# Optimization experiments

Measured on AMD Instinct MI355X. Metric: run time of the kernel, lower is better.

## Reference

```python
import jax, jax.numpy as jnp
import numpy as np

N_NODES = 50000
N_EDGES = 400000
IN_CH = 109
OUT_CH = 32


def setup_inputs() -> dict:
    key = jax.random.key(0)
    ks = jax.random.split(key, 12)
    dims = [(IN_CH, 10 * OUT_CH), (10 * OUT_CH, 2 * OUT_CH), (2 * OUT_CH, OUT_CH), (2 * OUT_CH, OUT_CH)]
    inp = {
        'x': jax.random.normal(ks[0], (N_NODES, IN_CH), dtype=jnp.float32),
        'edge_index': jax.random.randint(ks[1], (2, N_EDGES), 0, N_NODES, dtype=jnp.int64) if jax.config.jax_enable_x64 else jax.random.randint(ks[1], (2, N_EDGES), 0, N_NODES, dtype=jnp.int32),
    }
    names = ['W1', 'b1', 'W2', 'b2', 'Wmu', 'bmu', 'Wls', 'bls']
    for i, (fi, fo) in enumerate(dims):
        scale = 1.0 / np.sqrt(fi)
        inp[names[2 * i]] = jax.random.uniform(ks[2 + 2 * i], (fi, fo), minval=-scale, maxval=scale, dtype=jnp.float32)
        inp[names[2 * i + 1]] = jnp.zeros((fo,), dtype=jnp.float32)
    return inp


def _gcn_conv(x, src, dst, norm, W, b, n):
    # PyG GCNConv: h = x @ W, then symmetric-normalized aggregation, then + b
    h = x @ W                                   # [N, F_out]
    msg = h[src] * norm[:, None]                # [E+N, F_out]
    out = jax.ops.segment_sum(msg, dst, num_segments=n)
    return out + b


def _norm_and_loops(edge_index, n):
    # add self loops, compute D^{-1/2}(A+I)D^{-1/2} edge weights
    loops = jnp.arange(n, dtype=edge_index.dtype)
    src = jnp.concatenate([edge_index[0], loops])
    dst = jnp.concatenate([edge_index[1], loops])
    deg = jax.ops.segment_sum(jnp.ones_like(src, dtype=jnp.float32), dst, num_segments=n)
    dinv = jnp.where(deg > 0, jax.lax.rsqrt(jnp.maximum(deg, 1.0)), 0.0)
    norm = dinv[src] * dinv[dst]
    return src, dst, norm


def reference(x, edge_index, W1, b1, W2, b2, Wmu, bmu, Wls, bls):
    n = x.shape[0]
    src, dst, norm = _norm_and_loops(edge_index, n)
    h = jax.nn.relu(_gcn_conv(x, src, dst, norm, W1, b1, n))
    h = jax.nn.relu(_gcn_conv(h, src, dst, norm, W2, b2, n))
    mu = _gcn_conv(h, src, dst, norm, Wmu, bmu, n)
    logstd = _gcn_conv(h, src, dst, norm, Wls, bls, n)
    return (mu, logstd)
```

## Files before the change

kernel.cpp:

```cpp
#include <hip/hip_runtime.h>

#define NN 50000
#define NE 400000

typedef __attribute__((ext_vector_type(8))) short short8v;
typedef __attribute__((ext_vector_type(4))) float f32x4;

__device__ __forceinline__ unsigned short f2bf_rtn(float x) {
    unsigned u = __float_as_uint(x);
    unsigned r = u + 0x7FFFu + ((u >> 16) & 1u);
    return (unsigned short)(r >> 16);
}
__device__ __forceinline__ float bf2f(unsigned short h) {
    return __uint_as_float(((unsigned)h) << 16);
}

__global__ void prep_kernel(const float* __restrict__ x,
                            const float* __restrict__ W1, const float* __restrict__ W2,
                            const float* __restrict__ Wmu, const float* __restrict__ Wls,
                            unsigned* __restrict__ xp, int* __restrict__ zero_base,
                            unsigned short* __restrict__ w1t_hi,
                            unsigned short* __restrict__ w2t_hi,
                            unsigned short* __restrict__ wct_hi) {
    int b = blockIdx.x, tid = threadIdx.x;
    if (b < 12500) {
        int idx = b * 256 + tid;
        int i = idx >> 6, c2 = (idx & 63) * 2;
        long xb = (long)i * 109;
        float v0 = (c2 < 109) ? x[xb + c2] : 0.0f;
        float v1 = (c2 + 1 < 109) ? x[xb + c2 + 1] : 0.0f;
        xp[idx] = (unsigned)f2bf_rtn(v0) | ((unsigned)f2bf_rtn(v1) << 16);
    } else if (b < 12891) {
        int i = (b - 12500) * 256 + tid;
        if (i < 100096) zero_base[i] = 0;
    } else if (b < 13051) {
        int idx = (b - 12891) * 256 + tid;
        int n = idx >> 7, k = idx & 127;
        float v = (k < 109) ? W1[(long)k * 320 + n] : 0.0f;
        w1t_hi[idx] = f2bf_rtn(v);
    } else if (b < 13131) {
        int idx = (b - 13051) * 256 + tid;
        int n = idx / 320, k = idx - n * 320;
        w2t_hi[idx] = f2bf_rtn(W2[(long)k * 64 + n]);
    } else {
        int idx = (b - 13131) * 256 + tid;
        int n = idx >> 6, k = idx & 63;
        float v = (n < 32) ? Wmu[k * 32 + n] : Wls[k * 32 + (n - 32)];
        wct_hi[idx] = f2bf_rtn(v);
    }
}

__global__ void hist_kernel(const int* __restrict__ dst, int* __restrict__ counts) {
    for (int e = blockIdx.x * blockDim.x + threadIdx.x; e < NE; e += gridDim.x * blockDim.x)
        atomicAdd(&counts[dst[e]], 1);
}

__global__ void dinv_scan1_kernel(const int* __restrict__ counts, float* __restrict__ dinv,
                                  int* __restrict__ rowstart, int* __restrict__ bsum) {
    __shared__ int tmp[256];
    int tid = threadIdx.x;
    int i = blockIdx.x * 256 + tid;
    int v = (i < NN) ? counts[i] : 0;
    if (i < NN) dinv[i] = rsqrtf((float)(v + 1));
    tmp[tid] = v;
    __syncthreads();
    for (int off = 1; off < 256; off <<= 1) {
        int t = 0;
        if (tid >= off) t = tmp[tid - off];
        __syncthreads();
        if (tid >= off) tmp[tid] += t;
        __syncthreads();
    }
    if (i < NN) rowstart[i] = tmp[tid] - v;
    if (tid == 255) bsum[blockIdx.x] = tmp[255];
}

__global__ void scan23_kernel(int* __restrict__ rowstart, const int* __restrict__ bsum) {
    __shared__ int red[4];
    int tid = threadIdx.x;
    int v = (tid < 196 && tid < (int)blockIdx.x) ? bsum[tid] : 0;
    for (int off = 32; off > 0; off >>= 1) v += __shfl_down(v, off, 64);
    if ((tid & 63) == 0) red[tid >> 6] = v;
    __syncthreads();
    int pref = red[0] + red[1] + red[2] + red[3];
    int i = blockIdx.x * 256 + tid;
    if (i < NN) rowstart[i] += pref;
    if (i == 0) rowstart[NN] = NE;
}

__global__ void scatter_kernel(const int* __restrict__ src, const int* __restrict__ dst,
                               const int* __restrict__ rowstart, int* __restrict__ cursor,
                               int* __restrict__ esrc) {
    for (int e = blockIdx.x * blockDim.x + threadIdx.x; e < NE; e += gridDim.x * blockDim.x) {
        int d = dst[e];
        int pos = rowstart[d] + atomicAdd(&cursor[d], 1);
        esrc[pos] = src[e];
    }
}

__global__ __launch_bounds__(256) void agg109_packed_kernel(const int* __restrict__ rowstart,
                                                            const int* __restrict__ esrc,
                                                            const float* __restrict__ dinv,
                                                            const unsigned* __restrict__ xp,
                                                            unsigned* __restrict__ xa_hi32) {
    int wave = blockIdx.x * (blockDim.x >> 6) + (threadIdx.x >> 6);
    if (wave >= NN) return;
    int lane = threadIdx.x & 63;
    float wd = dinv[wave];
    unsigned pself = xp[(long)wave * 64 + lane];
    float acc0 = __uint_as_float(pself << 16) * wd;
    float acc1 = __uint_as_float(pself & 0xFFFF0000u) * wd;
    int j0 = rowstart[wave], j1 = rowstart[wave + 1];
    int j = j0;
    for (; j + 8 <= j1; j += 8) {
        int s[8];
        float w[8];
        unsigned pp[8];
        #pragma unroll
        for (int u = 0; u < 8; ++u) s[u] = esrc[j + u];
        #pragma unroll
        for (int u = 0; u < 8; ++u) w[u] = dinv[s[u]];
        #pragma unroll
        for (int u = 0; u < 8; ++u) pp[u] = xp[(long)s[u] * 64 + lane];
        #pragma unroll
        for (int u = 0; u < 8; ++u) {
            acc0 = fmaf(__uint_as_float(pp[u] << 16), w[u], acc0);
            acc1 = fmaf(__uint_as_float(pp[u] & 0xFFFF0000u), w[u], acc1);
        }
    }
    for (; j + 4 <= j1; j += 4) {
        int s0 = esrc[j], s1 = esrc[j + 1], s2 = esrc[j + 2], s3 = esrc[j + 3];
        float w0 = dinv[s0], w1 = dinv[s1], w2 = dinv[s2], w3 = dinv[s3];
        unsigned p0 = xp[(long)s0 * 64 + lane], p1 = xp[(long)s1 * 64 + lane];
        unsigned p2 = xp[(long)s2 * 64 + lane], p3 = xp[(long)s3 * 64 + lane];
        acc0 = fmaf(__uint_as_float(p0 << 16), w0, acc0);
        acc1 = fmaf(__uint_as_float(p0 & 0xFFFF0000u), w0, acc1);
        acc0 = fmaf(__uint_as_float(p1 << 16), w1, acc0);
        acc1 = fmaf(__uint_as_float(p1 & 0xFFFF0000u), w1, acc1);
        acc0 = fmaf(__uint_as_float(p2 << 16), w2, acc0);
        acc1 = fmaf(__uint_as_float(p2 & 0xFFFF0000u), w2, acc1);
        acc0 = fmaf(__uint_as_float(p3 << 16), w3, acc0);
        acc1 = fmaf(__uint_as_float(p3 & 0xFFFF0000u), w3, acc1);
    }
    for (; j < j1; ++j) {
        int s = esrc[j];
        float w = dinv[s];
        unsigned pv = xp[(long)s * 64 + lane];
        acc0 = fmaf(__uint_as_float(pv << 16), w, acc0);
        acc1 = fmaf(__uint_as_float(pv & 0xFFFF0000u), w, acc1);
    }
    acc0 *= wd;
    acc1 *= wd;
    xa_hi32[(long)wave * 64 + lane] =
        (unsigned)f2bf_rtn(acc0) | ((unsigned)f2bf_rtn(acc1) << 16);
}

__global__ __launch_bounds__(256) void agg64_relu_bf16_kernel(const int* __restrict__ rowstart,
                                                              const int* __restrict__ esrc,
                                                              const float* __restrict__ dinv,
                                                              const unsigned short* __restrict__ g,
                                                              const float* __restrict__ b,
                                                              unsigned short* __restrict__ hhi) {
    int wave = blockIdx.x * (blockDim.x >> 6) + (threadIdx.x >> 6);
    if (wave >= NN) return;
    int lane = threadIdx.x & 63;
    long base = (long)wave * 64;
    float acc = bf2f(g[base + lane]);
    int j0 = rowstart[wave], j1 = rowstart[wave + 1];
    int j = j0;
    for (; j + 8 <= j1; j += 8) {
        int s[8];
        float pp[8];
        #pragma unroll
        for (int u = 0; u < 8; ++u) s[u] = esrc[j + u];
        #pragma unroll
        for (int u = 0; u < 8; ++u) pp[u] = bf2f(g[(long)s[u] * 64 + lane]);
        #pragma unroll
        for (int u = 0; u < 8; ++u) acc += pp[u];
    }
    for (; j + 4 <= j1; j += 4) {
        int s0 = esrc[j], s1 = esrc[j + 1], s2 = esrc[j + 2], s3 = esrc[j + 3];
        float p0 = bf2f(g[(long)s0 * 64 + lane]), p1 = bf2f(g[(long)s1 * 64 + lane]);
        float p2 = bf2f(g[(long)s2 * 64 + lane]), p3 = bf2f(g[(long)s3 * 64 + lane]);
        acc += p0 + p1 + p2 + p3;
    }
    for (; j < j1; ++j) acc += bf2f(g[(long)esrc[j] * 64 + lane]);
    float v = acc * dinv[wave] + b[lane];
    v = v > 0.0f ? v : 0.0f;
    hhi[base + lane] = f2bf_rtn(v);
}

#define LDT 72
__global__ __launch_bounds__(1024) void agg_gemm3_kernel(const int* __restrict__ rowstart,
                                                         const int* __restrict__ esrc,
                                                         const float* __restrict__ dinv,
                                                         const unsigned short* __restrict__ h,
                                                         const unsigned short* __restrict__ wct_hi,
                                                         const float* __restrict__ bmu,
                                                         const float* __restrict__ bls,
                                                         float* __restrict__ out) {
    __shared__ unsigned short As[64 * LDT];
    __shared__ unsigned short Bs[64 * LDT];
    int tid = threadIdx.x;
    int wid = tid >> 6, lane = tid & 63;
    int m0 = blockIdx.x * 64;

    if (tid < 512) {
        int row = tid >> 3, slot = tid & 7;
        *(uint4*)&Bs[row * LDT + slot * 8] = *(const uint4*)&wct_hi[row * 64 + slot * 8];
    }

    #pragma unroll
    for (int t = 0; t < 4; ++t) {
        int node = m0 + wid * 4 + t;
        int i = node < NN ? node : NN - 1;
        long base = (long)i * 64;
        float wd = dinv[i];
        float acc = bf2f(h[base + lane]) * wd;
        int j0 = rowstart[i], j1 = rowstart[i + 1];
        int j = j0;
        for (; j + 8 <= j1; j += 8) {
            int s[8];
            float w[8], pp[8];
            #pragma unroll
            for (int u = 0; u < 8; ++u) s[u] = esrc[j + u];
            #pragma unroll
            for (int u = 0; u < 8; ++u) w[u] = dinv[s[u]];
            #pragma unroll
            for (int u = 0; u < 8; ++u) pp[u] = bf2f(h[(long)s[u] * 64 + lane]);
            #pragma unroll
            for (int u = 0; u < 8; ++u) acc = fmaf(pp[u], w[u], acc);
        }
        for (; j + 4 <= j1; j += 4) {
            int s0 = esrc[j], s1 = esrc[j + 1], s2 = esrc[j + 2], s3 = esrc[j + 3];
            float w0 = dinv[s0], w1 = dinv[s1], w2 = dinv[s2], w3 = dinv[s3];
            float p0 = bf2f(h[(long)s0 * 64 + lane]), p1 = bf2f(h[(long)s1 * 64 + lane]);
            float p2 = bf2f(h[(long)s2 * 64 + lane]), p3 = bf2f(h[(long)s3 * 64 + lane]);
            acc = fmaf(p0, w0, acc); acc = fmaf(p1, w1, acc);
            acc = fmaf(p2, w2, acc); acc = fmaf(p3, w3, acc);
        }
        for (; j < j1; ++j) {
            int s = esrc[j];
            acc = fmaf(bf2f(h[(long)s * 64 + lane]), dinv[s], acc);
        }
        As[(wid * 4 + t) * LDT + lane] = f2bf_rtn(acc * wd);
    }
    __syncthreads();

    int r = wid >> 2, c = wid & 3;
    int l15 = lane & 15, l4 = lane >> 4;
    f32x4 acc4 = {};
    #pragma unroll
    for (int ks = 0; ks < 2; ++ks) {
        int koff = ks * 32 + l4 * 8;
        short8v ah = *(const short8v*)&As[(r * 16 + l15) * LDT + koff];
        short8v bh = *(const short8v*)&Bs[(c * 16 + l15) * LDT + koff];
        acc4 = __builtin_amdgcn_mfma_f32_16x16x32_bf16(ah, bh, acc4, 0, 0, 0);
    }
    int rbase = m0 + r * 16 + l4 * 4;
    int gcol = c * 16 + l15;
    #pragma unroll
    for (int q2 = 0; q2 < 4; ++q2) {
        int grow = rbase + q2;
        if (grow >= NN) continue;
        float v = acc4[q2];
        if (gcol < 32)
            out[(long)grow * 32 + gcol] = v + bmu[gcol];
        else
            out[(long)NN * 32 + (long)grow * 32 + (gcol - 32)] = v + bls[gcol - 32];
    }
}

template <int MODE>
__global__ __launch_bounds__(256) void mfma_gemm_kernel(
    const unsigned short* __restrict__ Ahi,
    const unsigned short* __restrict__ Bhi,
    const float* __restrict__ bias,
    const float* __restrict__ dinv,
    unsigned short* __restrict__ Chi, int M, int N, int K, int grid_n) {
    __shared__ unsigned short As[64 * LDT];
    __shared__ unsigned short Bs[64 * LDT];
    int tid = threadIdx.x;
    int wid = tid >> 6, lane = tid & 63;
    int l15 = lane & 15, l4 = lane >> 4;

    int T = gridDim.x;
    int xcd = blockIdx.x & 7, jj = blockIdx.x >> 3;
    int q = T >> 3, r = T & 7;
    int start = (xcd < r) ? xcd * (q + 1) : r * (q + 1) + (xcd - r) * q;
    int lin = start + jj;
    int bm = lin / grid_n, bn = lin - bm * grid_n;
    int bm0 = bm * 64, bn0 = bn * 64;

    f32x4 acc[4] = {};

    for (int kc = 0; kc < K; kc += 64) {
        #pragma unroll
        for (int r2 = 0; r2 < 2; ++r2) {
            int idx = tid + 256 * r2;
            int row = idx >> 3, slot = idx & 7;
            int grow = bm0 + row;
            if (grow >= M) grow = M - 1;
            long go = (long)grow * K + kc + slot * 8;
            *(uint4*)&As[row * LDT + slot * 8] = *(const uint4*)&Ahi[go];
            long gob = (long)(bn0 + row) * K + kc + slot * 8;
            *(uint4*)&Bs[row * LDT + slot * 8] = *(const uint4*)&Bhi[gob];
        }
        __syncthreads();
        #pragma unroll
        for (int ks = 0; ks < 2; ++ks) {
            int koff = ks * 32 + l4 * 8;
            int ra = (wid * 16 + l15) * LDT + koff;
            short8v ah = *(const short8v*)&As[ra];
            #pragma unroll
            for (int n = 0; n < 4; ++n) {
                int rb = (n * 16 + l15) * LDT + koff;
                short8v bh = *(const short8v*)&Bs[rb];
                acc[n] = __builtin_amdgcn_mfma_f32_16x16x32_bf16(ah, bh, acc[n], 0, 0, 0);
            }
        }
        __syncthreads();
    }
    int rbase = bm0 + wid * 16 + l4 * 4;
    #pragma unroll
    for (int q2 = 0; q2 < 4; ++q2) {
        int grow = rbase + q2;
        if (grow >= M) continue;
        float rs = (MODE == 1) ? dinv[grow] : 0.0f;
        #pragma unroll
        for (int n = 0; n < 4; ++n) {
            int gcol = bn0 + n * 16 + l15;
            float v = acc[n][q2];
            if (MODE == 0) {
                v += bias[gcol];
                v = v > 0.0f ? v : 0.0f;
                Chi[(long)grow * N + gcol] = f2bf_rtn(v);
            } else {
                Chi[(long)grow * N + gcol] = f2bf_rtn(v * rs);
            }
        }
    }
}

extern "C" void kernel_launch(void* const* d_in, const int* in_sizes, int n_in,
                              void* d_out, int out_size, void* d_ws, size_t ws_size,
                              hipStream_t stream) {
    const float* x   = (const float*)d_in[0];
    const int*   ei  = (const int*)d_in[1];
    const int*   src = ei;
    const int*   dst = ei + NE;
    const float* W1  = (const float*)d_in[2];
    const float* b1  = (const float*)d_in[3];
    const float* W2  = (const float*)d_in[4];
    const float* b2  = (const float*)d_in[5];
    const float* Wmu = (const float*)d_in[6];
    const float* bmu = (const float*)d_in[7];
    const float* Wls = (const float*)d_in[8];
    const float* bls = (const float*)d_in[9];
    float* out = (float*)d_out;

    char* p = (char*)d_ws;
    float* dinv   = (float*)p; p += 50048 * 4;
    int* counts   = (int*)p;   p += 50048 * 4;
    int* cursor   = (int*)p;   p += 50048 * 4;
    int* rowstart = (int*)p;   p += 50056 * 4;
    int* bsum     = (int*)p;   p += 256 * 4;
    int* esrc     = (int*)p;   p += 400000 * 4;
    unsigned* xp          = (unsigned*)p;       p += 50000L * 64 * 4;
    unsigned short* xa_hi = (unsigned short*)p; p += 50000L * 128 * 2;
    unsigned short* g2b   = (unsigned short*)p; p += 50000L * 64 * 2;
    unsigned short* h1_hi = (unsigned short*)p; p += 50000L * 320 * 2;
    unsigned short* w1t_hi = (unsigned short*)p; p += 320 * 128 * 2;
    unsigned short* w2t_hi = (unsigned short*)p; p += 64 * 320 * 2;
    unsigned short* wct_hi = (unsigned short*)p; p += 64 * 64 * 2;
    unsigned short* h2_hi = xa_hi;

    const int TB = 256;
    const int NB_NODES = (NN + TB - 1) / TB;
    const int NB_AGG = (NN * 64 + TB - 1) / TB;

    prep_kernel<<<13147, TB, 0, stream>>>(x, W1, W2, Wmu, Wls, xp, counts,
                                          w1t_hi, w2t_hi, wct_hi);
    hist_kernel<<<1024, TB, 0, stream>>>(dst, counts);
    dinv_scan1_kernel<<<NB_NODES, TB, 0, stream>>>(counts, dinv, rowstart, bsum);
    scan23_kernel<<<NB_NODES, TB, 0, stream>>>(rowstart, bsum);
    scatter_kernel<<<1024, TB, 0, stream>>>(src, dst, rowstart, cursor, esrc);

    agg109_packed_kernel<<<NB_AGG, TB, 0, stream>>>(rowstart, esrc, dinv, xp,
                                                    (unsigned*)xa_hi);
    mfma_gemm_kernel<0><<<782 * 5, 256, 0, stream>>>(xa_hi, w1t_hi, b1, nullptr,
                                                     h1_hi, NN, 320, 128, 5);

    mfma_gemm_kernel<1><<<782, 256, 0, stream>>>(h1_hi, w2t_hi, nullptr, dinv,
                                                 g2b, NN, 64, 320, 1);
    agg64_relu_bf16_kernel<<<NB_AGG, TB, 0, stream>>>(rowstart, esrc, dinv, g2b, b2, h2_hi);

    agg_gemm3_kernel<<<782, 1024, 0, stream>>>(rowstart, esrc, dinv, h2_hi, wct_hi,
                                               bmu, bls, out);
}
```

Before: 166.4 us.

## Fuse layer-1 and layer-2 GEMMs, keeping hidden activations in LDS

Replaces the two separate MFMA GEMM launches with one kernel. For each 64-row tile it computes relu(xa@W1+b1) across all 320 columns into shared memory, then immediately multiplies that by W2 and scales by dinv. This removes the 50000x320 bf16 intermediate round-trip through global memory and one launch. In exchange it uses about 76 KB of LDS per block, which lowers occupancy, and each block now runs the N-chunks serially, so there are fewer blocks doing more work each.

```diff
diff --git a/kernel.cpp b/kernel.cpp
--- a/kernel.cpp
+++ b/kernel.cpp
@@ -155,6 +155,116 @@
         (unsigned)f2bf_rtn(acc0) | ((unsigned)f2bf_rtn(acc1) << 16);
 }
 
+#define LDA_T 136
+#define LDH 328
+
+__global__ __launch_bounds__(256) void gemm12_kernel(const unsigned short* __restrict__ xa,
+                                                     const unsigned short* __restrict__ w1t,
+                                                     const unsigned short* __restrict__ w2t,
+                                                     const float* __restrict__ b1,
+                                                     const float* __restrict__ dinv,
+                                                     unsigned short* __restrict__ g2b) {
+    __shared__ unsigned short As[64 * LDA_T];
+    __shared__ unsigned short Bs[64 * LDA_T];
+    __shared__ unsigned short Hs[64 * LDH];
+    int tid = threadIdx.x;
+    int wid = tid >> 6, lane = tid & 63;
+    int l15 = lane & 15, l4 = lane >> 4;
+
+    int T = gridDim.x;
+    int xcd = blockIdx.x & 7, jj = blockIdx.x >> 3;
+    int q = T >> 3, r = T & 7;
+    int start = (xcd < r) ? xcd * (q + 1) : r * (q + 1) + (xcd - r) * q;
+    int bm0 = (start + jj) * 64;
+
+    #pragma unroll
+    for (int r2 = 0; r2 < 4; ++r2) {
+        int idx = tid + 256 * r2;
+        int row = idx >> 4, slot = idx & 15;
+        int grow = bm0 + row;
+        if (grow >= NN) grow = NN - 1;
+        *(uint4*)&As[row * LDA_T + slot * 8] = *(const uint4*)&xa[(long)grow * 128 + slot * 8];
+    }
+    #pragma unroll
+    for (int r2 = 0; r2 < 4; ++r2) {
+        int idx = tid + 256 * r2;
+        int row = idx >> 4, slot = idx & 15;
+        *(uint4*)&Bs[row * LDA_T + slot * 8] = *(const uint4*)&w1t[(long)row * 128 + slot * 8];
+    }
+    __syncthreads();
+
+    for (int nc = 0; nc < 5; ++nc) {
+        f32x4 acc[4] = {};
+        #pragma unroll
+        for (int ks = 0; ks < 4; ++ks) {
+            int koff = ks * 32 + l4 * 8;
+            short8v ah = *(const short8v*)&As[(wid * 16 + l15) * LDA_T + koff];
+            #pragma unroll
+            for (int n = 0; n < 4; ++n) {
+                short8v bh = *(const short8v*)&Bs[(n * 16 + l15) * LDA_T + koff];
+                acc[n] = __builtin_amdgcn_mfma_f32_16x16x32_bf16(ah, bh, acc[n], 0, 0, 0);
+            }
+        }
+        int rbase = wid * 16 + l4 * 4;
+        #pragma unroll
+        for (int q2 = 0; q2 < 4; ++q2) {
+            #pragma unroll
+            for (int n = 0; n < 4; ++n) {
+                int gcol = nc * 64 + n * 16 + l15;
+                float v = acc[n][q2] + b1[gcol];
+                v = v > 0.0f ? v : 0.0f;
+                Hs[(rbase + q2) * LDH + gcol] = f2bf_rtn(v);
+            }
+        }
+        __syncthreads();
+        if (nc < 4) {
+            #pragma unroll
+            for (int r2 = 0; r2 < 4; ++r2) {
+                int idx = tid + 256 * r2;
+                int row = idx >> 4, slot = idx & 15;
+                *(uint4*)&Bs[row * LDA_T + slot * 8] =
+                    *(const uint4*)&w1t[(long)(nc * 64 + 64 + row) * 128 + slot * 8];
+            }
+            __syncthreads();
+        }
+    }
+
+    f32x4 acc2[4] = {};
+    for (int kc = 0; kc < 5; ++kc) {
+        #pragma unroll
+        for (int r2 = 0; r2 < 2; ++r2) {
+            int idx = tid + 256 * r2;
+            int row = idx >> 3, slot = idx & 7;
+            *(uint4*)&Bs[row * LDA_T + slot * 8] =
+                *(const uint4*)&w2t[(long)row * 320 + kc * 64 + slot * 8];
+        }
+        __syncthreads();
+        #pragma unroll
+        for (int ks = 0; ks < 2; ++ks) {
+            int koff = ks * 32 + l4 * 8;
+            short8v ah = *(const short8v*)&Hs[(wid * 16 + l15) * LDH + kc * 64 + koff];
+            #pragma unroll
+            for (int n = 0; n < 4; ++n) {
+                short8v bh = *(const short8v*)&Bs[(n * 16 + l15) * LDA_T + koff];
+                acc2[n] = __builtin_amdgcn_mfma_f32_16x16x32_bf16(ah, bh, acc2[n], 0, 0, 0);
+            }
+        }
+        __syncthreads();
+    }
+    int rbase = bm0 + wid * 16 + l4 * 4;
+    #pragma unroll
+    for (int q2 = 0; q2 < 4; ++q2) {
+        int grow = rbase + q2;
+        if (grow >= NN) continue;
+        float rs = dinv[grow];
+        #pragma unroll
+        for (int n = 0; n < 4; ++n) {
+            int gcol = n * 16 + l15;
+            g2b[(long)grow * 64 + gcol] = f2bf_rtn(acc2[n][q2] * rs);
+        }
+    }
+}
+
 __global__ __launch_bounds__(256) void agg64_relu_bf16_kernel(const int* __restrict__ rowstart,
                                                               const int* __restrict__ esrc,
                                                               const float* __restrict__ dinv,
@@ -271,77 +381,6 @@
     }
 }
 
-template <int MODE>
-__global__ __launch_bounds__(256) void mfma_gemm_kernel(
-    const unsigned short* __restrict__ Ahi,
-    const unsigned short* __restrict__ Bhi,
-    const float* __restrict__ bias,
-    const float* __restrict__ dinv,
-    unsigned short* __restrict__ Chi, int M, int N, int K, int grid_n) {
-    __shared__ unsigned short As[64 * LDT];
-    __shared__ unsigned short Bs[64 * LDT];
-    int tid = threadIdx.x;
-    int wid = tid >> 6, lane = tid & 63;
-    int l15 = lane & 15, l4 = lane >> 4;
-
-    int T = gridDim.x;
-    int xcd = blockIdx.x & 7, jj = blockIdx.x >> 3;
-    int q = T >> 3, r = T & 7;
-    int start = (xcd < r) ? xcd * (q + 1) : r * (q + 1) + (xcd - r) * q;
-    int lin = start + jj;
-    int bm = lin / grid_n, bn = lin - bm * grid_n;
-    int bm0 = bm * 64, bn0 = bn * 64;
-
-    f32x4 acc[4] = {};
-
-    for (int kc = 0; kc < K; kc += 64) {
-        #pragma unroll
-        for (int r2 = 0; r2 < 2; ++r2) {
-            int idx = tid + 256 * r2;
-            int row = idx >> 3, slot = idx & 7;
-            int grow = bm0 + row;
-            if (grow >= M) grow = M - 1;
-            long go = (long)grow * K + kc + slot * 8;
-            *(uint4*)&As[row * LDT + slot * 8] = *(const uint4*)&Ahi[go];
-            long gob = (long)(bn0 + row) * K + kc + slot * 8;
-            *(uint4*)&Bs[row * LDT + slot * 8] = *(const uint4*)&Bhi[gob];
-        }
-        __syncthreads();
-        #pragma unroll
-        for (int ks = 0; ks < 2; ++ks) {
-            int koff = ks * 32 + l4 * 8;
-            int ra = (wid * 16 + l15) * LDT + koff;
-            short8v ah = *(const short8v*)&As[ra];
-            #pragma unroll
-            for (int n = 0; n < 4; ++n) {
-                int rb = (n * 16 + l15) * LDT + koff;
-                short8v bh = *(const short8v*)&Bs[rb];
-                acc[n] = __builtin_amdgcn_mfma_f32_16x16x32_bf16(ah, bh, acc[n], 0, 0, 0);
-            }
-        }
-        __syncthreads();
-    }
-    int rbase = bm0 + wid * 16 + l4 * 4;
-    #pragma unroll
-    for (int q2 = 0; q2 < 4; ++q2) {
-        int grow = rbase + q2;
-        if (grow >= M) continue;
-        float rs = (MODE == 1) ? dinv[grow] : 0.0f;
-        #pragma unroll
-        for (int n = 0; n < 4; ++n) {
-            int gcol = bn0 + n * 16 + l15;
-            float v = acc[n][q2];
-            if (MODE == 0) {
-                v += bias[gcol];
-                v = v > 0.0f ? v : 0.0f;
-                Chi[(long)grow * N + gcol] = f2bf_rtn(v);
-            } else {
-                Chi[(long)grow * N + gcol] = f2bf_rtn(v * rs);
-            }
-        }
-    }
-}
-
 extern "C" void kernel_launch(void* const* d_in, const int* in_sizes, int n_in,
                               void* d_out, int out_size, void* d_ws, size_t ws_size,
                               hipStream_t stream) {
@@ -369,7 +408,6 @@
     unsigned* xp          = (unsigned*)p;       p += 50000L * 64 * 4;
     unsigned short* xa_hi = (unsigned short*)p; p += 50000L * 128 * 2;
     unsigned short* g2b   = (unsigned short*)p; p += 50000L * 64 * 2;
-    unsigned short* h1_hi = (unsigned short*)p; p += 50000L * 320 * 2;
     unsigned short* w1t_hi = (unsigned short*)p; p += 320 * 128 * 2;
     unsigned short* w2t_hi = (unsigned short*)p; p += 64 * 320 * 2;
     unsigned short* wct_hi = (unsigned short*)p; p += 64 * 64 * 2;
@@ -388,11 +426,9 @@
 
     agg109_packed_kernel<<<NB_AGG, TB, 0, stream>>>(rowstart, esrc, dinv, xp,
                                                     (unsigned*)xa_hi);
-    mfma_gemm_kernel<0><<<782 * 5, 256, 0, stream>>>(xa_hi, w1t_hi, b1, nullptr,
-                                                     h1_hi, NN, 320, 128, 5);
-
-    mfma_gemm_kernel<1><<<782, 256, 0, stream>>>(h1_hi, w2t_hi, nullptr, dinv,
-                                                 g2b, NN, 64, 320, 1);
+
+    gemm12_kernel<<<782, 256, 0, stream>>>(xa_hi, w1t_hi, w2t_hi, b1, dinv, g2b);
+
     agg64_relu_bf16_kernel<<<NB_AGG, TB, 0, stream>>>(rowstart, esrc, dinv, g2b, b2, h2_hi);
 
     agg_gemm3_kernel<<<782, 1024, 0, stream>>>(rowstart, esrc, dinv, h2_hi, wct_hi,
```

New measurement: 158.7 us, median of 3. 1.05x faster.
